# Kernel optimization log

Hardware: AMD Instinct MI355X
Metric: run time of the kernel (lower is better)

The kernel has to match this reference:

```python
import jax, jax.numpy as jnp
import numpy as np

B, N = 16, 1024
NT = 2    # atom types (Ni, Pt)
NPT = 3   # pair types: NiNi, NiPt, PtPt


def setup_inputs() -> dict:
    key = jax.random.key(0)
    k1, k2 = jax.random.split(key, 2)
    types = jax.random.randint(k1, (B, N, 1), 0, NT, dtype=jnp.int32)
    # interatomic distances in [1.5, 9.0] Angstrom, symmetric, self-distance pushed beyond cutoff
    r = 1.5 + 7.5 * jax.random.uniform(k2, (B, N, N, 1), dtype=jnp.float32)
    r = 0.5 * (r + jnp.swapaxes(r, 1, 2))
    eye = jnp.eye(N, dtype=bool)[None, :, :, None]
    distances = jnp.where(eye, 100.0, r)
    # pair type index for combinations_with_replacement ordering: (0,0)->0,(0,1)->1,(1,1)->2
    t_i = types[:, :, None, 0]
    t_j = types[:, None, :, 0]
    tmin = jnp.minimum(t_i, t_j)
    tmax = jnp.maximum(t_i, t_j)
    pair_types = (tmin * NT - (tmin * (tmin - 1)) // 2 + (tmax - tmin))[..., None].astype(jnp.int32)
    # learned parameters, one per pair type (Gupta/RGL-style EAM)
    A = jnp.array([0.20, 0.25, 0.30], jnp.float32)       # pair repulsion prefactor
    p = jnp.array([9.0, 10.0, 11.0], jnp.float32)        # pair repulsion decay
    xi = jnp.array([1.5, 1.8, 2.1], jnp.float32)         # hopping integral
    q = jnp.array([2.7, 3.0, 3.3], jnp.float32)          # density decay
    r0 = jnp.array([2.49, 2.63, 2.77], jnp.float32)      # equilibrium NN distance
    cut_a = jnp.full((NPT,), 5.0, jnp.float32)           # cutoff onset
    cut_b = jnp.full((NPT,), 7.5, jnp.float32)           # cutoff end
    # per-atom-type embedding scale and energy offset
    emb_scale = jnp.array([1.0, 1.1], jnp.float32)
    offset = jnp.array([-0.01, 0.02], jnp.float32)
    return dict(distances=distances, A=A, p=p, xi=xi, q=q, r0=r0,
                cut_a=cut_a, cut_b=cut_b, emb_scale=emb_scale, offset=offset,
                types=types, pair_types=pair_types)


def reference(distances, A, p, xi, q, r0, cut_a, cut_b, emb_scale, offset, types, pair_types):
    # dense_where body: route every pair by its pair type. The per-pair-type layers
    # share one functional family, so the where-loop is equivalent to a parameter gather.
    pt = pair_types[..., 0]          # [B,N,N] int
    r = distances[..., 0]            # [B,N,N]
    a = cut_a[pt]
    b = cut_b[pt]
    x = (r - a) / (b - a)
    # polynomial cutoff: 1 for r<a, 0 for r>b, cubic smoothstep in between
    fcut = jnp.where(r < a, 1.0, jnp.where(r > b, 0.0, 1.0 - 3.0 * x**2 + 2.0 * x**3))
    rn = r / r0[pt] - 1.0            # InputNormalizationAndShift
    phi = A[pt] * jnp.exp(-p[pt] * rn) * fcut          # pair potential
    rho = xi[pt]**2 * jnp.exp(-2.0 * q[pt] * rn) * fcut  # pair density
    sum_phi = jnp.sum(phi, axis=2)   # [B,N] sum over neighbors j (axis=-2 of [...,N,1])
    sum_rho = jnp.sum(rho, axis=2)   # [B,N]
    t = types[..., 0]                # [B,N]
    # embedding energy F_t(rho) = -s_t * sqrt(rho) plus per-type offset
    emb = -emb_scale[t] * jnp.sqrt(sum_rho) + offset[t]
    atomic_energies = 0.5 * sum_phi + emb
    energy = jnp.sum(atomic_energies, axis=1, keepdims=True)  # [B,1]
    n_atoms = jnp.sum((t >= 0).astype(energy.dtype), axis=1, keepdims=True)
    energy_per_atom = energy / n_atoms
    return jnp.concatenate([energy, energy_per_atom], axis=-1)  # [B,2]
```

## Files before the change

### kernel.cpp

```cpp
#include <hip/hip_runtime.h>
#include <math.h>

#define NATOMS 1024
#define NBATCH 16

__global__ __launch_bounds__(256) void eam_row_kernel(
    const float* __restrict__ distances,
    const float* __restrict__ A,   const float* __restrict__ p,
    const float* __restrict__ xi,  const float* __restrict__ q,
    const float* __restrict__ r0,  const float* __restrict__ cut_a,
    const float* __restrict__ cut_b,
    const float* __restrict__ emb_scale, const float* __restrict__ offset,
    const int* __restrict__ types,
    float* __restrict__ ws)
{
    __shared__ int   lds_t[NATOMS];
    __shared__ float red[8];

    const int row = blockIdx.x;
    const int b   = row >> 10;
    const int i   = row & (NATOMS - 1);
    const int tid = threadIdx.x;

    reinterpret_cast<int4*>(lds_t)[tid] =
        reinterpret_cast<const int4*>(types + b * NATOMS)[tid];
    __syncthreads();

    const int t_i = lds_t[i];

    const int kA = t_i;
    const int kB = t_i + 1;

    const float CaA = A[kA] * __expf(p[kA]);
    const float CbA = -(p[kA] / r0[kA]);
    const float CcA = xi[kA] * xi[kA] * __expf(2.0f * q[kA]);
    const float CdA = -(2.0f * q[kA] / r0[kA]);
    const float ibaA = 1.0f / (cut_b[kA] - cut_a[kA]);
    const float xoA  = -cut_a[kA] * ibaA;

    const float CaB = A[kB] * __expf(p[kB]);
    const float CbB = -(p[kB] / r0[kB]);
    const float CcB = xi[kB] * xi[kB] * __expf(2.0f * q[kB]);
    const float CdB = -(2.0f * q[kB] / r0[kB]);
    const float ibaB = 1.0f / (cut_b[kB] - cut_a[kB]);
    const float xoB  = -cut_a[kB] * ibaB;

    const float4 d4 = reinterpret_cast<const float4*>(
        distances + (size_t)row * NATOMS)[tid];
    const int4 t4 = reinterpret_cast<const int4*>(lds_t)[tid];

    float sphi = 0.0f, srho = 0.0f;

    const float rr[4] = {d4.x, d4.y, d4.z, d4.w};
    const int   tt[4] = {t4.x, t4.y, t4.z, t4.w};
#pragma unroll
    for (int c = 0; c < 4; ++c) {
        const float r  = rr[c];
        const bool  sB = (tt[c] != 0);
        const float Ca  = sB ? CaB  : CaA;
        const float Cb  = sB ? CbB  : CbA;
        const float Cc  = sB ? CcB  : CcA;
        const float Cd  = sB ? CdB  : CdA;
        const float iba = sB ? ibaB : ibaA;
        const float xo  = sB ? xoB  : xoA;

        const float x    = fmaf(r, iba, xo);
        const float xc   = fminf(fmaxf(x, 0.0f), 1.0f);
        const float fcut = fmaf(xc * xc, fmaf(2.0f, xc, -3.0f), 1.0f);
        const float e1   = __expf(Cb * r);
        const float e2   = __expf(Cd * r);
        sphi = fmaf(Ca * e1, fcut, sphi);
        srho = fmaf(Cc * e2, fcut, srho);
    }

#pragma unroll
    for (int off = 32; off; off >>= 1) {
        sphi += __shfl_down(sphi, off);
        srho += __shfl_down(srho, off);
    }
    const int wave = tid >> 6;
    if ((tid & 63) == 0) {
        red[wave * 2]     = sphi;
        red[wave * 2 + 1] = srho;
    }
    __syncthreads();
    if (tid == 0) {
        const float SP = red[0] + red[2] + red[4] + red[6];
        const float SR = red[1] + red[3] + red[5] + red[7];
        const float e  = 0.5f * SP - emb_scale[t_i] * sqrtf(SR) + offset[t_i];
        ws[row] = e;
    }
}

__global__ __launch_bounds__(256) void eam_reduce_kernel(
    const float* __restrict__ ws, float* __restrict__ out)
{
    __shared__ float red[4];
    const int b   = blockIdx.x;
    const int tid = threadIdx.x;

    const float4 v = reinterpret_cast<const float4*>(ws + b * NATOMS)[tid];
    float s = (v.x + v.y) + (v.z + v.w);
#pragma unroll
    for (int off = 32; off; off >>= 1) s += __shfl_down(s, off);
    if ((tid & 63) == 0) red[tid >> 6] = s;
    __syncthreads();
    if (tid == 0) {
        const float E = (red[0] + red[1]) + (red[2] + red[3]);
        out[b * 2]     = E;
        out[b * 2 + 1] = E * (1.0f / (float)NATOMS);
    }
}

extern "C" void kernel_launch(void* const* d_in, const int* in_sizes, int n_in,
                              void* d_out, int out_size, void* d_ws, size_t ws_size,
                              hipStream_t stream) {
    const float* distances = (const float*)d_in[0];
    const float* A         = (const float*)d_in[1];
    const float* p         = (const float*)d_in[2];
    const float* xi        = (const float*)d_in[3];
    const float* q         = (const float*)d_in[4];
    const float* r0        = (const float*)d_in[5];
    const float* cut_a     = (const float*)d_in[6];
    const float* cut_b     = (const float*)d_in[7];
    const float* emb_scale = (const float*)d_in[8];
    const float* offset    = (const float*)d_in[9];
    const int*   types     = (const int*)d_in[10];

    float* ws  = (float*)d_ws;
    float* out = (float*)d_out;

    eam_row_kernel<<<NBATCH * NATOMS, 256, 0, stream>>>(
        distances, A, p, xi, q, r0, cut_a, cut_b, emb_scale, offset, types, ws);
    eam_reduce_kernel<<<NBATCH, 256, 0, stream>>>(ws, out);
}
```

Before: 162.2 us.

## Assign one wavefront per row and fold prefactors into exp2 exponents

Each 256-thread block now handles four rows, one per wavefront, so the types array is staged into LDS once per four rows. The cross-wave LDS reduction and second barrier go away, and there are four times fewer blocks. The amplitude prefactors are folded into the exponent as log2 offsets and evaluated with the hardware exp2 builtin, which removes two multiplies per pair. Folding the prefactors this way slightly changes floating-point rounding.

```diff
diff --git a/kernel.cpp b/kernel.cpp
--- a/kernel.cpp
+++ b/kernel.cpp
@@ -3,6 +3,7 @@
 
 #define NATOMS 1024
 #define NBATCH 16
+#define ROWS_PER_BLOCK 4
 
 __global__ __launch_bounds__(256) void eam_row_kernel(
     const float* __restrict__ distances,
@@ -14,63 +15,72 @@
     const int* __restrict__ types,
     float* __restrict__ ws)
 {
-    __shared__ int   lds_t[NATOMS];
-    __shared__ float red[8];
+    __shared__ int lds_t[NATOMS];
 
-    const int row = blockIdx.x;
-    const int b   = row >> 10;
-    const int i   = row & (NATOMS - 1);
-    const int tid = threadIdx.x;
+    const int tid  = threadIdx.x;
+    const int row0 = blockIdx.x * ROWS_PER_BLOCK;
+    const int b    = row0 >> 10;
 
     reinterpret_cast<int4*>(lds_t)[tid] =
         reinterpret_cast<const int4*>(types + b * NATOMS)[tid];
     __syncthreads();
 
+    const int w   = tid >> 6;
+    const int l   = tid & 63;
+    const int row = row0 + w;
+    const int i   = row & (NATOMS - 1);
     const int t_i = lds_t[i];
 
+    const float L2E = 1.4426950408889634f;
     const int kA = t_i;
     const int kB = t_i + 1;
 
-    const float CaA = A[kA] * __expf(p[kA]);
-    const float CbA = -(p[kA] / r0[kA]);
-    const float CcA = xi[kA] * xi[kA] * __expf(2.0f * q[kA]);
-    const float CdA = -(2.0f * q[kA] / r0[kA]);
+    const float GpA = -p[kA] * L2E / r0[kA];
+    const float LpA = log2f(A[kA]) + p[kA] * L2E;
+    const float GrA = -2.0f * q[kA] * L2E / r0[kA];
+    const float LrA = 2.0f * (log2f(xi[kA]) + q[kA] * L2E);
     const float ibaA = 1.0f / (cut_b[kA] - cut_a[kA]);
     const float xoA  = -cut_a[kA] * ibaA;
 
-    const float CaB = A[kB] * __expf(p[kB]);
-    const float CbB = -(p[kB] / r0[kB]);
-    const float CcB = xi[kB] * xi[kB] * __expf(2.0f * q[kB]);
-    const float CdB = -(2.0f * q[kB] / r0[kB]);
+    const float GpB = -p[kB] * L2E / r0[kB];
+    const float LpB = log2f(A[kB]) + p[kB] * L2E;
+    const float GrB = -2.0f * q[kB] * L2E / r0[kB];
+    const float LrB = 2.0f * (log2f(xi[kB]) + q[kB] * L2E);
     const float ibaB = 1.0f / (cut_b[kB] - cut_a[kB]);
     const float xoB  = -cut_a[kB] * ibaB;
 
-    const float4 d4 = reinterpret_cast<const float4*>(
-        distances + (size_t)row * NATOMS)[tid];
-    const int4 t4 = reinterpret_cast<const int4*>(lds_t)[tid];
+    const float4* drow = reinterpret_cast<const float4*>(
+        distances + (size_t)row * NATOMS);
+    const int4* trow = reinterpret_cast<const int4*>(lds_t);
 
     float sphi = 0.0f, srho = 0.0f;
 
-    const float rr[4] = {d4.x, d4.y, d4.z, d4.w};
-    const int   tt[4] = {t4.x, t4.y, t4.z, t4.w};
 #pragma unroll
-    for (int c = 0; c < 4; ++c) {
-        const float r  = rr[c];
-        const bool  sB = (tt[c] != 0);
-        const float Ca  = sB ? CaB  : CaA;
-        const float Cb  = sB ? CbB  : CbA;
-        const float Cc  = sB ? CcB  : CcA;
-        const float Cd  = sB ? CdB  : CdA;
-        const float iba = sB ? ibaB : ibaA;
-        const float xo  = sB ? xoB  : xoA;
+    for (int it = 0; it < 4; ++it) {
+        const float4 d4 = drow[it * 64 + l];
+        const int4   t4 = trow[it * 64 + l];
 
-        const float x    = fmaf(r, iba, xo);
-        const float xc   = fminf(fmaxf(x, 0.0f), 1.0f);
-        const float fcut = fmaf(xc * xc, fmaf(2.0f, xc, -3.0f), 1.0f);
-        const float e1   = __expf(Cb * r);
-        const float e2   = __expf(Cd * r);
-        sphi = fmaf(Ca * e1, fcut, sphi);
-        srho = fmaf(Cc * e2, fcut, srho);
+        const float rr[4] = {d4.x, d4.y, d4.z, d4.w};
+        const int   tt[4] = {t4.x, t4.y, t4.z, t4.w};
+#pragma unroll
+        for (int c = 0; c < 4; ++c) {
+            const float r  = rr[c];
+            const bool  sB = (tt[c] != 0);
+            const float Gp  = sB ? GpB  : GpA;
+            const float Lp  = sB ? LpB  : LpA;
+            const float Gr  = sB ? GrB  : GrA;
+            const float Lr  = sB ? LrB  : LrA;
+            const float iba = sB ? ibaB : ibaA;
+            const float xo  = sB ? xoB  : xoA;
+
+            const float e1 = __builtin_amdgcn_exp2f(fmaf(Gp, r, Lp));
+            const float e2 = __builtin_amdgcn_exp2f(fmaf(Gr, r, Lr));
+            const float x  = fmaf(r, iba, xo);
+            const float xc = fminf(fmaxf(x, 0.0f), 1.0f);
+            const float fc = fmaf(xc * xc, fmaf(2.0f, xc, -3.0f), 1.0f);
+            sphi = fmaf(e1, fc, sphi);
+            srho = fmaf(e2, fc, srho);
+        }
     }
 
 #pragma unroll
@@ -78,16 +88,8 @@
         sphi += __shfl_down(sphi, off);
         srho += __shfl_down(srho, off);
     }
-    const int wave = tid >> 6;
-    if ((tid & 63) == 0) {
-        red[wave * 2]     = sphi;
-        red[wave * 2 + 1] = srho;
-    }
-    __syncthreads();
-    if (tid == 0) {
-        const float SP = red[0] + red[2] + red[4] + red[6];
-        const float SR = red[1] + red[3] + red[5] + red[7];
-        const float e  = 0.5f * SP - emb_scale[t_i] * sqrtf(SR) + offset[t_i];
+    if (l == 0) {
+        const float e = 0.5f * sphi - emb_scale[t_i] * sqrtf(srho) + offset[t_i];
         ws[row] = e;
     }
 }
@@ -130,7 +132,7 @@
     float* ws  = (float*)d_ws;
     float* out = (float*)d_out;
 
-    eam_row_kernel<<<NBATCH * NATOMS, 256, 0, stream>>>(
+    eam_row_kernel<<<(NBATCH * NATOMS) / ROWS_PER_BLOCK, 256, 0, stream>>>(
         distances, A, p, xi, q, r0, cut_a, cut_b, emb_scale, offset, types, ws);
     eam_reduce_kernel<<<NBATCH, 256, 0, stream>>>(ws, out);
 }
```

Result: faster. 152.8 us (-5.8%).
